# Kernel optimization log

Measured on AMD Instinct MI355X. Metric: run time of the kernel, lower is better.

## Reference

```python
import jax, jax.numpy as jnp
import numpy as np

B, S, T = 512, 1024, 48  # batch, seq_len, num_tags


def setup_inputs() -> dict:
    key = jax.random.key(0)
    k1, k2, k3, k4, k5, k6 = jax.random.split(key, 6)
    emissions = jax.random.normal(k1, (B, S, T), dtype=jnp.float32)
    tags = jax.random.randint(k2, (B, S), 0, T)
    lengths = jax.random.randint(k3, (B,), 1, S + 1)
    mask = jnp.arange(S)[None, :] < lengths[:, None]  # contiguous prefix mask, bool
    # learned parameters (nn.Parameter zeros init in the module; use small random here)
    start_transitions = 0.01 * jax.random.normal(k4, (T,), dtype=jnp.float32)
    end_transitions = 0.01 * jax.random.normal(k5, (T,), dtype=jnp.float32)
    transitions = 0.01 * jax.random.normal(k6, (T, T), dtype=jnp.float32)
    return {
        "emissions": emissions,
        "tags": tags,
        "mask": mask,
        "start_transitions": start_transitions,
        "end_transitions": end_transitions,
        "transitions": transitions,
    }


def _log_partition(emissions, mask, start_transitions, end_transitions, transitions):
    # score[b, i] = log-sum over paths ending in tag i (note: this repo indexes
    # transitions[i, j] with j = previous tag inside the partition recursion).
    score0 = start_transitions[None, :] + emissions[:, 0]  # (B, T)

    def step(score, xs):
        emit_t, mask_t = xs  # (B, T), (B,)
        # score_t[b, i] = logsumexp_j(score[b, j] + transitions[i, j]) + emit_t[b, i]
        score_t = jax.nn.logsumexp(score[:, None, :] + transitions[None, :, :], axis=2) + emit_t
        score = jnp.where(mask_t[:, None], score_t, score)
        return score, None

    em = jnp.swapaxes(emissions[:, 1:], 0, 1)  # (S-1, B, T)
    mk = jnp.swapaxes(mask[:, 1:], 0, 1)       # (S-1, B)
    score, _ = jax.lax.scan(step, score0, (em, mk))
    return jax.nn.logsumexp(score + end_transitions[None, :], axis=1)  # (B,)


def _score_sentence(emissions, tags, mask, start_transitions, end_transitions, transitions):
    Bb = emissions.shape[0]
    bidx = jnp.arange(Bb)
    maskf = mask.astype(emissions.dtype)
    score = start_transitions[tags[:, 0]] + emissions[bidx, 0, tags[:, 0]]  # (B,)
    trans_sc = transitions[tags[:, :-1], tags[:, 1:]]  # (B, S-1)
    emit_sc = jnp.take_along_axis(emissions, tags[:, :, None], axis=2)[..., 0]  # (B, S)
    score = score + jnp.sum((trans_sc + emit_sc[:, 1:]) * maskf[:, 1:], axis=1)
    last_idx = jnp.sum(mask.astype(jnp.int32), axis=1) - 1  # (B,)
    last_tags = jnp.take_along_axis(tags, last_idx[:, None], axis=1)[:, 0]
    return score + end_transitions[last_tags]


def reference(emissions, tags, mask, start_transitions, end_transitions, transitions):
    log_denominator = _log_partition(emissions, mask, start_transitions, end_transitions, transitions)
    log_numerator = _score_sentence(emissions, tags, mask, start_transitions, end_transitions, transitions)
    return jnp.mean(log_denominator - log_numerator)
```

## Files before the change

### kernel.cpp

```cpp
#include <hip/hip_runtime.h>

#define BB 512
#define SS 1024
#define TT 48
#define GG 16
#define CK 8
#define NSLOT 4

typedef __attribute__((ext_vector_type(8))) short short8;
typedef __attribute__((ext_vector_type(4))) float float4v;
typedef unsigned uint2v __attribute__((ext_vector_type(2)));

__device__ __forceinline__ unsigned short f2bf(float x) {
    unsigned u = __float_as_uint(x);
    u += 0x7FFFu + ((u >> 16) & 1u);
    return (unsigned short)(u >> 16);
}
__device__ __forceinline__ unsigned pk2bf(float lo, float hi) {
#if __has_builtin(__builtin_amdgcn_cvt_pk_bf16_f32)
    typedef __bf16 bf16x2 __attribute__((ext_vector_type(2)));
    union { bf16x2 v; unsigned u; } cv;
    cv.v = __builtin_amdgcn_cvt_pk_bf16_f32(lo, hi);
    return cv.u;
#else
    return __builtin_amdgcn_perm(__float_as_uint(hi) + 0x8000u,
                                 __float_as_uint(lo) + 0x8000u, 0x07060302u);
#endif
}
__device__ __forceinline__ float wave_sum(float v) {
#pragma unroll
    for (int off = 32; off >= 1; off >>= 1) v += __shfl_xor(v, off, 64);
    return v;
}
__device__ __forceinline__ int wave_sum_i(int v) {
#pragma unroll
    for (int off = 32; off >= 1; off >>= 1) v += __shfl_xor(v, off, 64);
    return v;
}
__device__ __forceinline__ float xgrp_max(float m) {
#if __has_builtin(__builtin_amdgcn_permlane16_swap) && __has_builtin(__builtin_amdgcn_permlane32_swap)
    uint2v a = __builtin_amdgcn_permlane16_swap(__float_as_uint(m), __float_as_uint(m), false, false);
    m = fmaxf(__uint_as_float(a[0]), __uint_as_float(a[1]));
    uint2v b = __builtin_amdgcn_permlane32_swap(__float_as_uint(m), __float_as_uint(m), false, false);
    m = fmaxf(__uint_as_float(b[0]), __uint_as_float(b[1]));
#else
    m = fmaxf(m, __shfl_xor(m, 16, 64));
    m = fmaxf(m, __shfl_xor(m, 32, 64));
#endif
    return m;
}
__device__ __forceinline__ float xgrp_sum(float m) {
#if __has_builtin(__builtin_amdgcn_permlane16_swap) && __has_builtin(__builtin_amdgcn_permlane32_swap)
    uint2v a = __builtin_amdgcn_permlane16_swap(__float_as_uint(m), __float_as_uint(m), false, false);
    m = __uint_as_float(a[0]) + __uint_as_float(a[1]);
    uint2v b = __builtin_amdgcn_permlane32_swap(__float_as_uint(m), __float_as_uint(m), false, false);
    m = __uint_as_float(b[0]) + __uint_as_float(b[1]);
#else
    m += __shfl_xor(m, 16, 64);
    m += __shfl_xor(m, 32, 64);
#endif
    return m;
}

__global__ __launch_bounds__(256)
void crf_numer(const float* __restrict__ em, const int* __restrict__ tags,
               const int* __restrict__ mask, const float* __restrict__ start_tr,
               const float* __restrict__ end_tr, const float* __restrict__ trans,
               float* __restrict__ numer, int* __restrict__ lenArr) {
    const int b = blockIdx.x, tid = threadIdx.x;
    const float* emb = em + (size_t)b * SS * TT;
    const int* tg = tags + (size_t)b * SS;
    const int* mk = mask + (size_t)b * SS;
    const int s0 = tid * 4;
    const int4 t4 = *(const int4*)(tg + s0);
    const int4 m4 = *(const int4*)(mk + s0);
    const int tprev = (tid == 0) ? 0 : tg[s0 - 1];
    int cnt = (m4.x != 0) + (m4.y != 0) + (m4.z != 0) + (m4.w != 0);
    float ns = 0.f;
    if (tid > 0 && m4.x) ns += trans[tprev * TT + t4.x] + emb[(size_t)s0 * TT + t4.x];
    if (m4.y) ns += trans[t4.x * TT + t4.y] + emb[(size_t)(s0 + 1) * TT + t4.y];
    if (m4.z) ns += trans[t4.y * TT + t4.z] + emb[(size_t)(s0 + 2) * TT + t4.z];
    if (m4.w) ns += trans[t4.z * TT + t4.w] + emb[(size_t)(s0 + 3) * TT + t4.w];
    float wsum = wave_sum(ns);
    int wcnt = wave_sum_i(cnt);
    __shared__ float sf[4]; __shared__ int si[4];
    if ((tid & 63) == 0) { sf[tid >> 6] = wsum; si[tid >> 6] = wcnt; }
    __syncthreads();
    if (tid == 0) {
        float tot = sf[0] + sf[1] + sf[2] + sf[3];
        int L = si[0] + si[1] + si[2] + si[3];
        int t0 = tg[0];
        tot += start_tr[t0] + emb[t0] + end_tr[tg[L - 1]];
        numer[b] = tot;
        lenArr[b] = L;
    }
}

__global__ __launch_bounds__(320, 1)
void crf_fwd(const float* __restrict__ em, const float* __restrict__ start_tr,
             const float* __restrict__ end_tr, const float* __restrict__ trans,
             const int* __restrict__ lenArr, float* __restrict__ denomArr) {
    __shared__ float4v ring[NSLOT * CK * 3 * 64];

    const int tid = threadIdx.x;
    const int wave = tid >> 6, lane = tid & 63;
    const int wgbase = blockIdx.x * GG;
    const float4v Zv = {0.f, 0.f, 0.f, 0.f};

    if (wave == 0) {
        __builtin_amdgcn_s_setprio(1);
        const int n = lane & 15, q = lane >> 4;
        const int bb = wgbase + n;

        short8 afr[3][2];
#pragma unroll
        for (int mt = 0; mt < 3; ++mt) {
            const int so = mt * 16 + n;
#pragma unroll
            for (int kt = 0; kt < 2; ++kt) {
                short8 a;
#pragma unroll
                for (int i = 0; i < 8; ++i) {
                    int si_;
                    if (kt == 0) si_ = (i < 4) ? (q * 4 + i) : (16 + q * 4 + (i - 4));
                    else         si_ = (i < 4) ? (32 + q * 4 + i) : -1;
                    a[i] = (si_ >= 0) ? (short)f2bf(__expf(trans[so * TT + si_])) : (short)0;
                }
                afr[mt][kt] = a;
            }
        }

        const float* em0 = em + (size_t)bb * SS * TT + q * 4;
        float4v p0, p1, p2;
        {
            float4v v0 = *(const float4v*)(em0);
            float4v v1 = *(const float4v*)(em0 + 16);
            float4v v2 = *(const float4v*)(em0 + 32);
            const int sb = q * 4;
#pragma unroll
            for (int r = 0; r < 4; ++r) {
                p0[r] = __expf(start_tr[sb + r] + v0[r]);
                p1[r] = __expf(start_tr[16 + sb + r] + v1[r]);
                p2[r] = __expf(start_tr[32 + sb + r] + v2[r]);
            }
        }

        const int len = lenArr[bb];
        int Lmax = len;
#pragma unroll
        for (int off = 1; off < 64; off <<= 1) {
            int o = __shfl_xor(Lmax, off, 64);
            Lmax = Lmax > o ? Lmax : o;
        }
        const int P = (Lmax + 6) >> 3;

        const bool cc0 = (len == 1);
        float4v dc0 = cc0 ? p0 : Zv, dc1 = cc0 ? p1 : Zv, dc2 = cc0 ? p2 : Zv;
        float lcap = 0.f, logscale = 0.f;

        for (int pp = -3; pp < P; ++pp) {
            if (pp >= 0) {
                const float4v* rp = ring + (size_t)(pp % NSLOT) * (CK * 3 * 64) + lane;
                float4v e0 = rp[0], e1 = rp[64], e2 = rp[128];
                const int lo = 8 * pp + 2, hi = 8 * pp + 9;
                const bool any = __ballot((len >= lo) & (len <= hi)) != 0ull;
#pragma unroll
                for (int u = 0; u < 8; ++u) {
                    union { short8 v; unsigned w[4]; } B0, B1;
                    B0.w[0] = pk2bf(p0[0], p0[1]); B0.w[1] = pk2bf(p0[2], p0[3]);
                    B0.w[2] = pk2bf(p1[0], p1[1]); B0.w[3] = pk2bf(p1[2], p1[3]);
                    B1.w[0] = pk2bf(p2[0], p2[1]); B1.w[1] = pk2bf(p2[2], p2[3]);
                    B1.w[2] = 0u; B1.w[3] = 0u;
                    float4v A0 = __builtin_amdgcn_mfma_f32_16x16x32_bf16(afr[0][0], B0.v, Zv, 0, 0, 0);
                    float4v A1 = __builtin_amdgcn_mfma_f32_16x16x32_bf16(afr[1][0], B0.v, Zv, 0, 0, 0);
                    float4v A2 = __builtin_amdgcn_mfma_f32_16x16x32_bf16(afr[2][0], B0.v, Zv, 0, 0, 0);
                    A0 = __builtin_amdgcn_mfma_f32_16x16x32_bf16(afr[0][1], B1.v, A0, 0, 0, 0);
                    A1 = __builtin_amdgcn_mfma_f32_16x16x32_bf16(afr[1][1], B1.v, A1, 0, 0, 0);
                    A2 = __builtin_amdgcn_mfma_f32_16x16x32_bf16(afr[2][1], B1.v, A2, 0, 0, 0);
                    float4v n0, n1, n2;
                    if (u < 7) {
                        n0 = rp[(u + 1) * 192];
                        n1 = rp[(u + 1) * 192 + 64];
                        n2 = rp[(u + 1) * 192 + 128];
                    }
                    p0 = A0 * e0; p1 = A1 * e1; p2 = A2 * e2;
                    if (any) {
                        const bool cc = (len == 8 * pp + u + 2);
                        dc0 = cc ? p0 : dc0; dc1 = cc ? p1 : dc1; dc2 = cc ? p2 : dc2;
                        lcap = cc ? logscale : lcap;
                    }
                    e0 = n0; e1 = n1; e2 = n2;
                    if (u == 7) {
                        float m = fmaxf(fmaxf(p0[0], p0[1]), fmaxf(p0[2], p0[3]));
                        m = fmaxf(m, fmaxf(fmaxf(p1[0], p1[1]), fmaxf(p1[2], p1[3])));
                        m = fmaxf(m, fmaxf(fmaxf(p2[0], p2[1]), fmaxf(p2[2], p2[3])));
                        m = fmaxf(xgrp_max(m), 1e-30f);
                        logscale += __logf(m);
                        const float rm = __builtin_amdgcn_rcpf(m);
                        p0 *= rm; p1 *= rm; p2 *= rm;
                    }
                }
            }
            __builtin_amdgcn_s_barrier();
        }

        float pe = 0.f;
        {
            const int sb = q * 4;
#pragma unroll
            for (int r = 0; r < 4; ++r) {
                pe = fmaf(dc0[r], __expf(end_tr[sb + r]), pe);
                pe = fmaf(dc1[r], __expf(end_tr[16 + sb + r]), pe);
                pe = fmaf(dc2[r], __expf(end_tr[32 + sb + r]), pe);
            }
        }
        pe = xgrp_sum(pe);
        if (lane < 16) denomArr[bb] = lcap + __logf(pe);

    } else {
        const int T = (wave - 1) >> 1;
        const int sub = (wave - 1) & 1;
        const int nb = lane & 15, q4 = lane >> 4;
        const int bb = wgbase + nb;
        const int len_v = lenArr[bb];
        int Lmax = len_v;
#pragma unroll
        for (int off = 1; off < 64; off <<= 1) {
            int o = __shfl_xor(Lmax, off, 64);
            Lmax = Lmax > o ? Lmax : o;
        }
        const int P = (Lmax + 6) >> 3;

        const float* emP = em + (size_t)bb * SS * TT + q4 * 4;
        float4 buf[12];
        const float4v Z4 = {0.f, 0.f, 0.f, 0.f};

        for (int pp = -3; pp < P; ++pp) {
            int cv = pp + 1;
            if (cv >= 0 && cv < P && (cv & 1) == T) {
                float4v* wp = ring + (size_t)(cv % NSLOT) * (CK * 3 * 64) + lane;
#pragma unroll
                for (int k = 0; k < 12; ++k) {
                    const int i = sub * 12 + k, u = i / 3, j = i % 3;
                    const int t = 1 + 8 * cv + u;
                    const bool live = t < len_v;
                    float4 v = buf[k];
                    float4v o;
                    o[0] = __expf(v.x); o[1] = __expf(v.y);
                    o[2] = __expf(v.z); o[3] = __expf(v.w);
                    o = live ? o : Z4;
                    wp[(size_t)(u * 3 + j) * 64] = o;
                }
            }
            int ci = pp + 3;
            if (ci < P && (ci & 1) == T) {
#pragma unroll
                for (int k = 0; k < 12; ++k) {
                    const int i = sub * 12 + k, u = i / 3, j = i % 3;
                    int t = 1 + 8 * ci + u; t = t < SS ? t : SS - 1;
                    buf[k] = *(const float4*)(emP + (size_t)t * TT + j * 16);
                }
            }
            __builtin_amdgcn_s_waitcnt(0xC07F);
            __builtin_amdgcn_s_barrier();
        }
    }
}

__global__ __launch_bounds__(64)
void crf_reduce(const float* __restrict__ denom, const float* __restrict__ numer,
                float* __restrict__ out) {
    int lane = threadIdx.x;
    float s = 0.f;
    for (int i = lane; i < BB; i += 64) s += denom[i] - numer[i];
    s = wave_sum(s);
    if (lane == 0) out[0] = s * (1.0f / (float)BB);
}

extern "C" void kernel_launch(void* const* d_in, const int* in_sizes, int n_in,
                              void* d_out, int out_size, void* d_ws, size_t ws_size,
                              hipStream_t stream) {
    const float* emissions = (const float*)d_in[0];
    const int*   tags      = (const int*)d_in[1];
    const int*   mask      = (const int*)d_in[2];
    const float* start_tr  = (const float*)d_in[3];
    const float* end_tr    = (const float*)d_in[4];
    const float* trans     = (const float*)d_in[5];

    char* ws = (char*)d_ws;
    float* denom = (float*)ws;
    float* numer = (float*)(ws + 2048);
    int*   lenA  = (int*)(ws + 4096);

    crf_numer<<<BB, 256, 0, stream>>>(emissions, tags, mask, start_tr, end_tr,
                                      trans, numer, lenA);
    crf_fwd<<<BB / GG, 320, 0, stream>>>(emissions, start_tr, end_tr, trans,
                                         lenA, denom);
    crf_reduce<<<1, 64, 0, stream>>>(denom, numer, (float*)d_out);
}
```

Baseline: 299.3 us.

## Split CRF forward recursion into parallel segment matrix products and combine

The sequential forward recursion is replaced by a parallel scan. Each batch element's sequence is cut into four 256-step segments, and one wave per segment multiplies a full 48x48 transfer matrix through its steps with MFMA, renormalising each column. A separate combine kernel then chains the segment matrices with the start vector. The numerator is also spread over four blocks per batch, with length computed in its own kernel. This breaks the long serial dependency chain so more waves run concurrently, at the cost of three times the MFMA work per step, extra workspace traffic for the matrices, and more kernel launches.

```diff
diff --git a/kernel.cpp b/kernel.cpp
--- a/kernel.cpp
+++ b/kernel.cpp
@@ -3,9 +3,8 @@
 #define BB 512
 #define SS 1024
 #define TT 48
-#define GG 16
-#define CK 8
-#define NSLOT 4
+#define NSEG 4
+#define SL 256
 
 typedef __attribute__((ext_vector_type(8))) short short8;
 typedef __attribute__((ext_vector_type(4))) float float4v;
@@ -35,6 +34,11 @@
 __device__ __forceinline__ int wave_sum_i(int v) {
 #pragma unroll
     for (int off = 32; off >= 1; off >>= 1) v += __shfl_xor(v, off, 64);
+    return v;
+}
+__device__ __forceinline__ float wave_max(float v) {
+#pragma unroll
+    for (int off = 32; off >= 1; off >>= 1) v = fmaxf(v, __shfl_xor(v, off, 64));
     return v;
 }
 __device__ __forceinline__ float xgrp_max(float m) {
@@ -49,230 +53,254 @@
 #endif
     return m;
 }
-__device__ __forceinline__ float xgrp_sum(float m) {
-#if __has_builtin(__builtin_amdgcn_permlane16_swap) && __has_builtin(__builtin_amdgcn_permlane32_swap)
-    uint2v a = __builtin_amdgcn_permlane16_swap(__float_as_uint(m), __float_as_uint(m), false, false);
-    m = __uint_as_float(a[0]) + __uint_as_float(a[1]);
-    uint2v b = __builtin_amdgcn_permlane32_swap(__float_as_uint(m), __float_as_uint(m), false, false);
-    m = __uint_as_float(b[0]) + __uint_as_float(b[1]);
-#else
-    m += __shfl_xor(m, 16, 64);
-    m += __shfl_xor(m, 32, 64);
-#endif
-    return m;
-}
 
 __global__ __launch_bounds__(256)
-void crf_numer(const float* __restrict__ em, const int* __restrict__ tags,
-               const int* __restrict__ mask, const float* __restrict__ start_tr,
-               const float* __restrict__ end_tr, const float* __restrict__ trans,
-               float* __restrict__ numer, int* __restrict__ lenArr) {
+void crf_len(const int* __restrict__ mask, int* __restrict__ lenArr) {
     const int b = blockIdx.x, tid = threadIdx.x;
+    const int4 m4 = *(const int4*)(mask + (size_t)b * SS + tid * 4);
+    int cnt = (m4.x != 0) + (m4.y != 0) + (m4.z != 0) + (m4.w != 0);
+    cnt = wave_sum_i(cnt);
+    __shared__ int si[4];
+    if ((tid & 63) == 0) si[tid >> 6] = cnt;
+    __syncthreads();
+    if (tid == 0) lenArr[b] = si[0] + si[1] + si[2] + si[3];
+}
+
+__global__ __launch_bounds__(256)
+void crf_numer2(const float* __restrict__ em, const int* __restrict__ tags,
+                const int* __restrict__ mask, const float* __restrict__ start_tr,
+                const float* __restrict__ end_tr, const float* __restrict__ trans,
+                const int* __restrict__ lenArr, float* __restrict__ numer4) {
+    const int b = blockIdx.x >> 2, tid = threadIdx.x;
+    const int s = (blockIdx.x & 3) * 256 + tid;
+    const int* tg = tags + (size_t)b * SS;
     const float* emb = em + (size_t)b * SS * TT;
-    const int* tg = tags + (size_t)b * SS;
-    const int* mk = mask + (size_t)b * SS;
-    const int s0 = tid * 4;
-    const int4 t4 = *(const int4*)(tg + s0);
-    const int4 m4 = *(const int4*)(mk + s0);
-    const int tprev = (tid == 0) ? 0 : tg[s0 - 1];
-    int cnt = (m4.x != 0) + (m4.y != 0) + (m4.z != 0) + (m4.w != 0);
+    const int tc = tg[s];
     float ns = 0.f;
-    if (tid > 0 && m4.x) ns += trans[tprev * TT + t4.x] + emb[(size_t)s0 * TT + t4.x];
-    if (m4.y) ns += trans[t4.x * TT + t4.y] + emb[(size_t)(s0 + 1) * TT + t4.y];
-    if (m4.z) ns += trans[t4.y * TT + t4.z] + emb[(size_t)(s0 + 2) * TT + t4.z];
-    if (m4.w) ns += trans[t4.z * TT + t4.w] + emb[(size_t)(s0 + 3) * TT + t4.w];
-    float wsum = wave_sum(ns);
-    int wcnt = wave_sum_i(cnt);
-    __shared__ float sf[4]; __shared__ int si[4];
-    if ((tid & 63) == 0) { sf[tid >> 6] = wsum; si[tid >> 6] = wcnt; }
+    if (s >= 1) {
+        if (mask[(size_t)b * SS + s])
+            ns = trans[tg[s - 1] * TT + tc] + emb[(size_t)s * TT + tc];
+    } else {
+        ns = start_tr[tc] + emb[tc] + end_tr[tg[lenArr[b] - 1]];
+    }
+    ns = wave_sum(ns);
+    __shared__ float sf[4];
+    if ((tid & 63) == 0) sf[tid >> 6] = ns;
     __syncthreads();
-    if (tid == 0) {
-        float tot = sf[0] + sf[1] + sf[2] + sf[3];
-        int L = si[0] + si[1] + si[2] + si[3];
-        int t0 = tg[0];
-        tot += start_tr[t0] + emb[t0] + end_tr[tg[L - 1]];
-        numer[b] = tot;
-        lenArr[b] = L;
-    }
-}
-
-__global__ __launch_bounds__(320, 1)
-void crf_fwd(const float* __restrict__ em, const float* __restrict__ start_tr,
-             const float* __restrict__ end_tr, const float* __restrict__ trans,
-             const int* __restrict__ lenArr, float* __restrict__ denomArr) {
-    __shared__ float4v ring[NSLOT * CK * 3 * 64];
+    if (tid == 0) numer4[blockIdx.x] = sf[0] + sf[1] + sf[2] + sf[3];
+}
+
+__global__ __launch_bounds__(256, 2)
+void crf_seg(const float* __restrict__ em, const float* __restrict__ trans,
+             const int* __restrict__ lenArr, float* __restrict__ Mws,
+             float* __restrict__ Lws) {
+    __shared__ float4v ebuf[4][2][96];
 
     const int tid = threadIdx.x;
-    const int wave = tid >> 6, lane = tid & 63;
-    const int wgbase = blockIdx.x * GG;
+    const int w = tid >> 6, lane = tid & 63;
+    const int b = blockIdx.x, s = w;
+    const int L = lenArr[b];
+    if (L < 2 + s * SL) return;
+
+    const int c = lane & 15, q = lane >> 4;
+    const int t_start = 1 + s * SL;
+    const int t_end = min(t_start + SL - 1, L - 1);
+    const int steps = t_end - t_start + 1;
+    const int nfull = steps >> 3, tail = steps & 7;
+    const int nch = nfull + (tail ? 1 : 0);
     const float4v Zv = {0.f, 0.f, 0.f, 0.f};
 
-    if (wave == 0) {
-        __builtin_amdgcn_s_setprio(1);
-        const int n = lane & 15, q = lane >> 4;
-        const int bb = wgbase + n;
-
-        short8 afr[3][2];
-#pragma unroll
-        for (int mt = 0; mt < 3; ++mt) {
-            const int so = mt * 16 + n;
-#pragma unroll
-            for (int kt = 0; kt < 2; ++kt) {
-                short8 a;
-#pragma unroll
-                for (int i = 0; i < 8; ++i) {
-                    int si_;
-                    if (kt == 0) si_ = (i < 4) ? (q * 4 + i) : (16 + q * 4 + (i - 4));
-                    else         si_ = (i < 4) ? (32 + q * 4 + i) : -1;
-                    a[i] = (si_ >= 0) ? (short)f2bf(__expf(trans[so * TT + si_])) : (short)0;
-                }
-                afr[mt][kt] = a;
+    short8 afr[3][2];
+#pragma unroll
+    for (int mt = 0; mt < 3; ++mt) {
+        const int so = mt * 16 + c;
+#pragma unroll
+        for (int kt = 0; kt < 2; ++kt) {
+            short8 a;
+#pragma unroll
+            for (int i = 0; i < 8; ++i) {
+                int si_;
+                if (kt == 0) si_ = (i < 4) ? (q * 4 + i) : (16 + q * 4 + (i - 4));
+                else         si_ = (i < 4) ? (32 + q * 4 + i) : -1;
+                a[i] = (si_ >= 0) ? (short)f2bf(__expf(trans[so * TT + si_])) : (short)0;
             }
-        }
-
-        const float* em0 = em + (size_t)bb * SS * TT + q * 4;
-        float4v p0, p1, p2;
-        {
-            float4v v0 = *(const float4v*)(em0);
-            float4v v1 = *(const float4v*)(em0 + 16);
-            float4v v2 = *(const float4v*)(em0 + 32);
-            const int sb = q * 4;
-#pragma unroll
-            for (int r = 0; r < 4; ++r) {
-                p0[r] = __expf(start_tr[sb + r] + v0[r]);
-                p1[r] = __expf(start_tr[16 + sb + r] + v1[r]);
-                p2[r] = __expf(start_tr[32 + sb + r] + v2[r]);
+            afr[mt][kt] = a;
+        }
+    }
+
+    float4v S[3][3];
+#pragma unroll
+    for (int mt = 0; mt < 3; ++mt)
+#pragma unroll
+        for (int nc = 0; nc < 3; ++nc)
+#pragma unroll
+            for (int r = 0; r < 4; ++r)
+                S[mt][nc][r] = (mt * 16 + q * 4 + r == nc * 16 + c) ? 1.f : 0.f;
+    float ls[3] = {0.f, 0.f, 0.f};
+
+    const float* emB = em + (size_t)b * SS * TT;
+    float4v* eb = &ebuf[w][0][0];
+
+    auto stage_issue = [&](int tb, float4v& g0, float4v& g1) {
+        int t0 = tb + lane / 12; t0 = t0 > 1023 ? 1023 : t0;
+        g0 = *(const float4v*)(emB + (size_t)t0 * TT + (lane % 12) * 4);
+        if (lane < 32) {
+            const int m1 = 64 + lane;
+            int t1 = tb + m1 / 12; t1 = t1 > 1023 ? 1023 : t1;
+            g1 = *(const float4v*)(emB + (size_t)t1 * TT + (m1 % 12) * 4);
+        }
+    };
+    auto stage_commit = [&](int slot, const float4v g0, const float4v g1) {
+        float4v o;
+        o[0] = __expf(g0[0]); o[1] = __expf(g0[1]); o[2] = __expf(g0[2]); o[3] = __expf(g0[3]);
+        eb[slot * 96 + lane] = o;
+        if (lane < 32) {
+            float4v o1;
+            o1[0] = __expf(g1[0]); o1[1] = __expf(g1[1]); o1[2] = __expf(g1[2]); o1[3] = __expf(g1[3]);
+            eb[slot * 96 + 64 + lane] = o1;
+        }
+    };
+
+    auto step = [&](const float4v e0, const float4v e1, const float4v e2) {
+        union { short8 v; unsigned wd[4]; } B0[3], B1[3];
+#pragma unroll
+        for (int nc = 0; nc < 3; ++nc) {
+            B0[nc].wd[0] = pk2bf(S[0][nc][0], S[0][nc][1]);
+            B0[nc].wd[1] = pk2bf(S[0][nc][2], S[0][nc][3]);
+            B0[nc].wd[2] = pk2bf(S[1][nc][0], S[1][nc][1]);
+            B0[nc].wd[3] = pk2bf(S[1][nc][2], S[1][nc][3]);
+            B1[nc].wd[0] = pk2bf(S[2][nc][0], S[2][nc][1]);
+            B1[nc].wd[1] = pk2bf(S[2][nc][2], S[2][nc][3]);
+            B1[nc].wd[2] = 0u; B1[nc].wd[3] = 0u;
+        }
+        float4v D[3][3];
+#pragma unroll
+        for (int nc = 0; nc < 3; ++nc)
+#pragma unroll
+            for (int mt = 0; mt < 3; ++mt)
+                D[mt][nc] = __builtin_amdgcn_mfma_f32_16x16x32_bf16(afr[mt][0], B0[nc].v, Zv, 0, 0, 0);
+#pragma unroll
+        for (int nc = 0; nc < 3; ++nc)
+#pragma unroll
+            for (int mt = 0; mt < 3; ++mt)
+                D[mt][nc] = __builtin_amdgcn_mfma_f32_16x16x32_bf16(afr[mt][1], B1[nc].v, D[mt][nc], 0, 0, 0);
+#pragma unroll
+        for (int nc = 0; nc < 3; ++nc) {
+            S[0][nc] = D[0][nc] * e0;
+            S[1][nc] = D[1][nc] * e1;
+            S[2][nc] = D[2][nc] * e2;
+        }
+    };
+
+    auto renorm = [&]() {
+#pragma unroll
+        for (int nc = 0; nc < 3; ++nc) {
+            float m = fmaxf(fmaxf(S[0][nc][0], S[0][nc][1]), fmaxf(S[0][nc][2], S[0][nc][3]));
+            m = fmaxf(m, fmaxf(fmaxf(S[1][nc][0], S[1][nc][1]), fmaxf(S[1][nc][2], S[1][nc][3])));
+            m = fmaxf(m, fmaxf(fmaxf(S[2][nc][0], S[2][nc][1]), fmaxf(S[2][nc][2], S[2][nc][3])));
+            m = fmaxf(xgrp_max(m), 1e-30f);
+            ls[nc] += __logf(m);
+            const float rm = __builtin_amdgcn_rcpf(m);
+            S[0][nc] *= rm; S[1][nc] *= rm; S[2][nc] *= rm;
+        }
+    };
+
+    {
+        float4v g0, g1;
+        stage_issue(t_start, g0, g1);
+        stage_commit(0, g0, g1);
+    }
+
+    int slot = 0;
+    for (int ch = 0; ch < nfull; ++ch) {
+        const bool pf = (ch + 1 < nch);
+        float4v g0, g1;
+        if (pf) stage_issue(t_start + (ch + 1) * 8, g0, g1);
+        const float4v* rp = eb + slot * 96;
+#pragma unroll
+        for (int u = 0; u < 8; ++u) {
+            const float4v e0 = rp[u * 12 + q];
+            const float4v e1 = rp[u * 12 + 4 + q];
+            const float4v e2 = rp[u * 12 + 8 + q];
+            step(e0, e1, e2);
+        }
+        renorm();
+        if (pf) stage_commit(slot ^ 1, g0, g1);
+        slot ^= 1;
+    }
+    if (tail) {
+        const float4v* rp = eb + slot * 96;
+        for (int i = 0; i < tail; ++i) {
+            const float4v e0 = rp[i * 12 + q];
+            const float4v e1 = rp[i * 12 + 4 + q];
+            const float4v e2 = rp[i * 12 + 8 + q];
+            step(e0, e1, e2);
+        }
+    }
+
+    float* Mout = Mws + ((size_t)b * NSEG + s) * (TT * TT);
+#pragma unroll
+    for (int mt = 0; mt < 3; ++mt)
+#pragma unroll
+        for (int r = 0; r < 4; ++r) {
+            const int row = mt * 16 + q * 4 + r;
+#pragma unroll
+            for (int nc = 0; nc < 3; ++nc)
+                Mout[row * TT + nc * 16 + c] = S[mt][nc][r];
+        }
+    if (q == 0) {
+        float* Lout = Lws + ((size_t)b * NSEG + s) * TT;
+        Lout[c] = ls[0]; Lout[16 + c] = ls[1]; Lout[32 + c] = ls[2];
+    }
+}
+
+__global__ __launch_bounds__(64)
+void crf_combine(const float* __restrict__ em, const float* __restrict__ start_tr,
+                 const float* __restrict__ end_tr, const int* __restrict__ lenArr,
+                 const float* __restrict__ Mws, const float* __restrict__ Lws,
+                 float* __restrict__ denomArr) {
+    const int b = blockIdx.x, j = threadIdx.x;
+    const bool act = j < TT;
+    const int L = lenArr[b];
+    float v = act ? __expf(start_tr[j] + em[(size_t)b * SS * TT + j]) : 0.f;
+    float lp = 0.f;
+    const int k = (L - 2) >> 8;
+    __shared__ float wsh[TT];
+    for (int s = 0; s <= k; ++s) {
+        const float Lc = act ? Lws[((size_t)b * NSEG + s) * TT + j] : -3e38f;
+        const float mx = wave_max(Lc);
+        const float wv = act ? v * __expf(Lc - mx) : 0.f;
+        if (act) wsh[j] = wv;
+        __syncthreads();
+        float acc = 0.f;
+        if (act) {
+            const float* Mr = Mws + (((size_t)b * NSEG + s) * TT + j) * TT;
+#pragma unroll
+            for (int t4i = 0; t4i < TT; t4i += 4) {
+                const float4 mm = *(const float4*)(Mr + t4i);
+                acc += mm.x * wsh[t4i] + mm.y * wsh[t4i + 1]
+                     + mm.z * wsh[t4i + 2] + mm.w * wsh[t4i + 3];
             }
         }
-
-        const int len = lenArr[bb];
-        int Lmax = len;
-#pragma unroll
-        for (int off = 1; off < 64; off <<= 1) {
-            int o = __shfl_xor(Lmax, off, 64);
-            Lmax = Lmax > o ? Lmax : o;
-        }
-        const int P = (Lmax + 6) >> 3;
-
-        const bool cc0 = (len == 1);
-        float4v dc0 = cc0 ? p0 : Zv, dc1 = cc0 ? p1 : Zv, dc2 = cc0 ? p2 : Zv;
-        float lcap = 0.f, logscale = 0.f;
-
-        for (int pp = -3; pp < P; ++pp) {
-            if (pp >= 0) {
-                const float4v* rp = ring + (size_t)(pp % NSLOT) * (CK * 3 * 64) + lane;
-                float4v e0 = rp[0], e1 = rp[64], e2 = rp[128];
-                const int lo = 8 * pp + 2, hi = 8 * pp + 9;
-                const bool any = __ballot((len >= lo) & (len <= hi)) != 0ull;
-#pragma unroll
-                for (int u = 0; u < 8; ++u) {
-                    union { short8 v; unsigned w[4]; } B0, B1;
-                    B0.w[0] = pk2bf(p0[0], p0[1]); B0.w[1] = pk2bf(p0[2], p0[3]);
-                    B0.w[2] = pk2bf(p1[0], p1[1]); B0.w[3] = pk2bf(p1[2], p1[3]);
-                    B1.w[0] = pk2bf(p2[0], p2[1]); B1.w[1] = pk2bf(p2[2], p2[3]);
-                    B1.w[2] = 0u; B1.w[3] = 0u;
-                    float4v A0 = __builtin_amdgcn_mfma_f32_16x16x32_bf16(afr[0][0], B0.v, Zv, 0, 0, 0);
-                    float4v A1 = __builtin_amdgcn_mfma_f32_16x16x32_bf16(afr[1][0], B0.v, Zv, 0, 0, 0);
-                    float4v A2 = __builtin_amdgcn_mfma_f32_16x16x32_bf16(afr[2][0], B0.v, Zv, 0, 0, 0);
-                    A0 = __builtin_amdgcn_mfma_f32_16x16x32_bf16(afr[0][1], B1.v, A0, 0, 0, 0);
-                    A1 = __builtin_amdgcn_mfma_f32_16x16x32_bf16(afr[1][1], B1.v, A1, 0, 0, 0);
-                    A2 = __builtin_amdgcn_mfma_f32_16x16x32_bf16(afr[2][1], B1.v, A2, 0, 0, 0);
-                    float4v n0, n1, n2;
-                    if (u < 7) {
-                        n0 = rp[(u + 1) * 192];
-                        n1 = rp[(u + 1) * 192 + 64];
-                        n2 = rp[(u + 1) * 192 + 128];
-                    }
-                    p0 = A0 * e0; p1 = A1 * e1; p2 = A2 * e2;
-                    if (any) {
-                        const bool cc = (len == 8 * pp + u + 2);
-                        dc0 = cc ? p0 : dc0; dc1 = cc ? p1 : dc1; dc2 = cc ? p2 : dc2;
-                        lcap = cc ? logscale : lcap;
-                    }
-                    e0 = n0; e1 = n1; e2 = n2;
-                    if (u == 7) {
-                        float m = fmaxf(fmaxf(p0[0], p0[1]), fmaxf(p0[2], p0[3]));
-                        m = fmaxf(m, fmaxf(fmaxf(p1[0], p1[1]), fmaxf(p1[2], p1[3])));
-                        m = fmaxf(m, fmaxf(fmaxf(p2[0], p2[1]), fmaxf(p2[2], p2[3])));
-                        m = fmaxf(xgrp_max(m), 1e-30f);
-                        logscale += __logf(m);
-                        const float rm = __builtin_amdgcn_rcpf(m);
-                        p0 *= rm; p1 *= rm; p2 *= rm;
-                    }
-                }
-            }
-            __builtin_amdgcn_s_barrier();
-        }
-
-        float pe = 0.f;
-        {
-            const int sb = q * 4;
-#pragma unroll
-            for (int r = 0; r < 4; ++r) {
-                pe = fmaf(dc0[r], __expf(end_tr[sb + r]), pe);
-                pe = fmaf(dc1[r], __expf(end_tr[16 + sb + r]), pe);
-                pe = fmaf(dc2[r], __expf(end_tr[32 + sb + r]), pe);
-            }
-        }
-        pe = xgrp_sum(pe);
-        if (lane < 16) denomArr[bb] = lcap + __logf(pe);
-
-    } else {
-        const int T = (wave - 1) >> 1;
-        const int sub = (wave - 1) & 1;
-        const int nb = lane & 15, q4 = lane >> 4;
-        const int bb = wgbase + nb;
-        const int len_v = lenArr[bb];
-        int Lmax = len_v;
-#pragma unroll
-        for (int off = 1; off < 64; off <<= 1) {
-            int o = __shfl_xor(Lmax, off, 64);
-            Lmax = Lmax > o ? Lmax : o;
-        }
-        const int P = (Lmax + 6) >> 3;
-
-        const float* emP = em + (size_t)bb * SS * TT + q4 * 4;
-        float4 buf[12];
-        const float4v Z4 = {0.f, 0.f, 0.f, 0.f};
-
-        for (int pp = -3; pp < P; ++pp) {
-            int cv = pp + 1;
-            if (cv >= 0 && cv < P && (cv & 1) == T) {
-                float4v* wp = ring + (size_t)(cv % NSLOT) * (CK * 3 * 64) + lane;
-#pragma unroll
-                for (int k = 0; k < 12; ++k) {
-                    const int i = sub * 12 + k, u = i / 3, j = i % 3;
-                    const int t = 1 + 8 * cv + u;
-                    const bool live = t < len_v;
-                    float4 v = buf[k];
-                    float4v o;
-                    o[0] = __expf(v.x); o[1] = __expf(v.y);
-                    o[2] = __expf(v.z); o[3] = __expf(v.w);
-                    o = live ? o : Z4;
-                    wp[(size_t)(u * 3 + j) * 64] = o;
-                }
-            }
-            int ci = pp + 3;
-            if (ci < P && (ci & 1) == T) {
-#pragma unroll
-                for (int k = 0; k < 12; ++k) {
-                    const int i = sub * 12 + k, u = i / 3, j = i % 3;
-                    int t = 1 + 8 * ci + u; t = t < SS ? t : SS - 1;
-                    buf[k] = *(const float4*)(emP + (size_t)t * TT + j * 16);
-                }
-            }
-            __builtin_amdgcn_s_waitcnt(0xC07F);
-            __builtin_amdgcn_s_barrier();
-        }
-    }
+        float m2 = fmaxf(wave_max(acc), 1e-30f);
+        v = act ? acc * __builtin_amdgcn_rcpf(m2) : 0.f;
+        lp += mx + __logf(m2);
+        __syncthreads();
+    }
+    const float contrib = act ? v * __expf(end_tr[j]) : 0.f;
+    const float tot = wave_sum(contrib);
+    if (j == 0) denomArr[b] = lp + __logf(tot);
 }
 
 __global__ __launch_bounds__(64)
-void crf_reduce(const float* __restrict__ denom, const float* __restrict__ numer,
-                float* __restrict__ out) {
-    int lane = threadIdx.x;
+void crf_reduce2(const float* __restrict__ denom, const float* __restrict__ numer4,
+                 float* __restrict__ out) {
+    const int lane = threadIdx.x;
     float s = 0.f;
-    for (int i = lane; i < BB; i += 64) s += denom[i] - numer[i];
+    for (int i = lane; i < BB; i += 64) {
+        const float n = numer4[4 * i] + numer4[4 * i + 1] + numer4[4 * i + 2] + numer4[4 * i + 3];
+        s += denom[i] - n;
+    }
     s = wave_sum(s);
     if (lane == 0) out[0] = s * (1.0f / (float)BB);
 }
@@ -288,13 +316,16 @@
     const float* trans     = (const float*)d_in[5];
 
     char* ws = (char*)d_ws;
-    float* denom = (float*)ws;
-    float* numer = (float*)(ws + 2048);
-    int*   lenA  = (int*)(ws + 4096);
-
-    crf_numer<<<BB, 256, 0, stream>>>(emissions, tags, mask, start_tr, end_tr,
-                                      trans, numer, lenA);
-    crf_fwd<<<BB / GG, 320, 0, stream>>>(emissions, start_tr, end_tr, trans,
-                                         lenA, denom);
-    crf_reduce<<<1, 64, 0, stream>>>(denom, numer, (float*)d_out);
-}
+    float* denom  = (float*)ws;
+    float* numer4 = (float*)(ws + 2048);
+    int*   lenA   = (int*)(ws + 10240);
+    float* Lws    = (float*)(ws + 12288);
+    float* Mws    = (float*)(ws + 405504);
+
+    crf_len<<<BB, 256, 0, stream>>>(mask, lenA);
+    crf_numer2<<<BB * 4, 256, 0, stream>>>(emissions, tags, mask, start_tr, end_tr,
+                                           trans, lenA, numer4);
+    crf_seg<<<BB, 256, 0, stream>>>(emissions, trans, lenA, Mws, Lws);
+    crf_combine<<<BB, 64, 0, stream>>>(emissions, start_tr, end_tr, lenA, Mws, Lws, denom);
+    crf_reduce2<<<1, 64, 0, stream>>>(denom, numer4, (float*)d_out);
+}
```

Result: slower. 306.0 us (+2.2%).
